# Kernel tuning notes

Measured on AMD Instinct MI355X. Metric: run time of the kernel, lower is better.

## Reference

```python
import jax, jax.numpy as jnp
import numpy as np

D_MODEL = 1024
NUM_HEADS = 16
HEAD_DIM = D_MODEL // NUM_HEADS


def setup_inputs() -> dict:
    key = jax.random.key(0)
    ks = jax.random.split(key, 9)
    s = 1.0 / np.sqrt(D_MODEL)
    return {
        "x": jax.random.normal(ks[0], (4, 2048, D_MODEL), dtype=jnp.float32),
        "Wq": jax.random.uniform(ks[1], (D_MODEL, D_MODEL), minval=-s, maxval=s, dtype=jnp.float32),
        "bq": jax.random.uniform(ks[2], (D_MODEL,), minval=-s, maxval=s, dtype=jnp.float32),
        "Wk": jax.random.uniform(ks[3], (D_MODEL, D_MODEL), minval=-s, maxval=s, dtype=jnp.float32),
        "bk": jax.random.uniform(ks[4], (D_MODEL,), minval=-s, maxval=s, dtype=jnp.float32),
        "Wv": jax.random.uniform(ks[5], (D_MODEL, D_MODEL), minval=-s, maxval=s, dtype=jnp.float32),
        "bv": jax.random.uniform(ks[6], (D_MODEL,), minval=-s, maxval=s, dtype=jnp.float32),
        "Wo": jax.random.uniform(ks[7], (D_MODEL, D_MODEL), minval=-s, maxval=s, dtype=jnp.float32),
        "bo": jax.random.uniform(ks[8], (D_MODEL,), minval=-s, maxval=s, dtype=jnp.float32),
    }


def reference(x, Wq, bq, Wk, bk, Wv, bv, Wo, bo):
    B, T, C = x.shape
    H, Dh = NUM_HEADS, HEAD_DIM
    # projections (nn.Linear applies x @ W^T + b)
    q = (x @ Wq.T + bq).reshape(B, T, H, Dh).transpose(0, 2, 1, 3)  # [B,H,T,Dh]
    k = (x @ Wk.T + bk).reshape(B, T, H, Dh).transpose(0, 2, 1, 3)
    v = (x @ Wv.T + bv).reshape(B, T, H, Dh).transpose(0, 2, 1, 3)
    scale = 1.0 / np.sqrt(Dh).astype(np.float32)
    att = jnp.einsum("bhqd,bhkd->bhqk", q, k) * scale  # [B,H,T,T]
    causal = jnp.tril(jnp.ones((T, T), dtype=bool))
    att = jnp.where(causal[None, None], att, -jnp.inf)
    att = jax.nn.softmax(att, axis=-1)
    # dropout is identity in eval mode
    out = jnp.einsum("bhqk,bhkd->bhqd", att, v)  # [B,H,T,Dh]
    out = out.transpose(0, 2, 1, 3).reshape(B, T, C)
    return out @ Wo.T + bo
```

## Files before the change

### kernel.cpp

```cpp
#include <hip/hip_runtime.h>
#include <stdint.h>

typedef __attribute__((ext_vector_type(8))) short short8;
typedef __attribute__((ext_vector_type(4))) short short4v;
typedef __attribute__((ext_vector_type(4))) float floatx4;

#define QSCALE 0.1803368801111f

__device__ __forceinline__ unsigned short f2bf(float f) {
  unsigned int u = __float_as_uint(f);
  unsigned int r = (u + 0x7FFFu + ((u >> 16) & 1u)) >> 16;
  return (unsigned short)r;
}

__device__ __forceinline__ unsigned int cvt_pk_bf16(float lo, float hi) {
  unsigned int r;
  asm("v_cvt_pk_bf16_f32 %0, %1, %2" : "=v"(r) : "v"(lo), "v"(hi));
  return r;
}

__device__ __forceinline__ void async_copy16(void* lds, const void* g) {
  __builtin_amdgcn_global_load_lds(
      (const __attribute__((address_space(1))) unsigned int*)g,
      (__attribute__((address_space(3))) unsigned int*)lds, 16, 0, 0);
}

__global__ __launch_bounds__(256) void f2b_kernel(const float* __restrict__ in,
                                                  unsigned short* __restrict__ out,
                                                  int n4) {
  int i = blockIdx.x * 256 + threadIdx.x;
  if (i >= n4) return;
  float4 v = ((const float4*)in)[i];
  short4v o;
  o[0] = (short)f2bf(v.x);
  o[1] = (short)f2bf(v.y);
  o[2] = (short)f2bf(v.z);
  o[3] = (short)f2bf(v.w);
  *(short4v*)(out + (long)i * 4) = o;
}

__global__ __launch_bounds__(256) void f2b4_kernel(
    const float* __restrict__ w0, const float* __restrict__ w1,
    const float* __restrict__ w2, const float* __restrict__ w3,
    unsigned short* __restrict__ o0, unsigned short* __restrict__ o1,
    unsigned short* __restrict__ o2, unsigned short* __restrict__ o3) {
  int which = blockIdx.x >> 10;
  const float* in = (which == 0) ? w0 : (which == 1) ? w1 : (which == 2) ? w2 : w3;
  unsigned short* out = (which == 0) ? o0 : (which == 1) ? o1 : (which == 2) ? o2 : o3;
  int i = (blockIdx.x & 1023) * 256 + threadIdx.x;
  float4 v = ((const float4*)in)[i];
  short4v o;
  o[0] = (short)f2bf(v.x);
  o[1] = (short)f2bf(v.y);
  o[2] = (short)f2bf(v.z);
  o[3] = (short)f2bf(v.w);
  *(short4v*)(out + (long)i * 4) = o;
}

__device__ __forceinline__ void gemm128_mainloop(
    const unsigned short* __restrict__ A, const unsigned short* __restrict__ Bt,
    int K, long brow, long bcol, unsigned short* As, unsigned short* Bs,
    floatx4 acc[4][4]) {
  const int tid = threadIdx.x;
  const int wave = tid >> 6;
  const int lane = tid & 63;
  const int wr = wave >> 1, wc = wave & 1;
  const int lr = lane & 15, lg = lane >> 4;

  const unsigned short* ga = A + (brow + (tid >> 2)) * (long)K + (tid & 3) * 8;
  const unsigned short* gb = Bt + (bcol + (tid >> 2)) * (long)K + (tid & 3) * 8;
  unsigned short* lA = As + wave * 512;
  unsigned short* lB = Bs + wave * 512;
  const int a_off = (wr * 64 + lr) * 32 + lg * 8;
  const int b_off = (wc * 64 + lr) * 32 + lg * 8;

  for (int kt = 0; kt < K; kt += 32) {
    __syncthreads();
    async_copy16(lA, ga);
    async_copy16(lA + 2048, ga + (long)64 * K);
    async_copy16(lB, gb);
    async_copy16(lB + 2048, gb + (long)64 * K);
    ga += 32;
    gb += 32;
    __syncthreads();
    short8 af[4], bf[4];
#pragma unroll
    for (int i = 0; i < 4; ++i) {
      af[i] = *(const short8*)(As + a_off + i * 512);
      bf[i] = *(const short8*)(Bs + b_off + i * 512);
    }
#pragma unroll
    for (int i = 0; i < 4; ++i)
#pragma unroll
      for (int j = 0; j < 4; ++j)
        acc[i][j] = __builtin_amdgcn_mfma_f32_16x16x32_bf16(af[i], bf[j], acc[i][j], 0, 0, 0);
  }
}

__global__ __launch_bounds__(256) void qkv_gemm(
    const unsigned short* __restrict__ xb, const unsigned short* __restrict__ wqkv,
    const float* __restrict__ bq, const float* __restrict__ bk,
    const float* __restrict__ bv, unsigned short* __restrict__ q_out,
    unsigned short* __restrict__ k_out, unsigned short* __restrict__ vt_out) {
  __shared__ unsigned short As[128 * 32];
  __shared__ unsigned short Bs[128 * 32];
  floatx4 zero = {0.f, 0.f, 0.f, 0.f};
  floatx4 acc[4][4];
#pragma unroll
  for (int i = 0; i < 4; ++i)
#pragma unroll
    for (int j = 0; j < 4; ++j) acc[i][j] = zero;

  long brow = (long)blockIdx.x * 128;
  long bcol = (long)blockIdx.y * 128;
  gemm128_mainloop(xb, wqkv, 1024, brow, bcol, As, Bs, acc);

  const int wave = threadIdx.x >> 6, lane = threadIdx.x & 63;
  const int wr = wave >> 1, wc = wave & 1, lr = lane & 15, lg = lane >> 4;
  const int kind = (int)(bcol >> 10);
  const float* bias = (kind == 0) ? bq : (kind == 1 ? bk : bv);
#pragma unroll
  for (int i = 0; i < 4; ++i)
#pragma unroll
    for (int j = 0; j < 4; ++j)
#pragma unroll
      for (int r = 0; r < 4; ++r) {
        int m = (int)brow + wr * 64 + i * 16 + lg * 4 + r;
        int n = (int)bcol + wc * 64 + j * 16 + lr;
        int f = n & 1023;
        float v = acc[i][j][r] + bias[f];
        if (kind == 0) v *= QSCALE;
        unsigned short o = f2bf(v);
        int h = f >> 6, d = f & 63;
        int b = m >> 11, t = m & 2047;
        long bh = (long)(b * 16 + h);
        if (kind == 0)
          q_out[(bh * 2048 + t) * 64 + d] = o;
        else if (kind == 1)
          k_out[(bh * 2048 + t) * 64 + d] = o;
        else
          vt_out[(bh * 64 + d) * 2048 + t] = o;
      }
}

__global__ __launch_bounds__(256) void out_gemm(
    const unsigned short* __restrict__ ob, const unsigned short* __restrict__ wo,
    const float* __restrict__ bo, float* __restrict__ out) {
  __shared__ unsigned short As[128 * 32];
  __shared__ unsigned short Bs[128 * 32];
  floatx4 zero = {0.f, 0.f, 0.f, 0.f};
  floatx4 acc[4][4];
#pragma unroll
  for (int i = 0; i < 4; ++i)
#pragma unroll
    for (int j = 0; j < 4; ++j) acc[i][j] = zero;

  long brow = (long)blockIdx.x * 128;
  long bcol = (long)blockIdx.y * 128;
  gemm128_mainloop(ob, wo, 1024, brow, bcol, As, Bs, acc);

  const int wave = threadIdx.x >> 6, lane = threadIdx.x & 63;
  const int wr = wave >> 1, wc = wave & 1, lr = lane & 15, lg = lane >> 4;
#pragma unroll
  for (int i = 0; i < 4; ++i)
#pragma unroll
    for (int j = 0; j < 4; ++j)
#pragma unroll
      for (int r = 0; r < 4; ++r) {
        int m = (int)brow + wr * 64 + i * 16 + lg * 4 + r;
        int n = (int)bcol + wc * 64 + j * 16 + lr;
        out[(long)m * 1024 + n] = acc[i][j][r] + bo[n];
      }
}

__device__ __forceinline__ void stage_kv(char* __restrict__ Kb, char* __restrict__ Vb,
                                         const char* __restrict__ Kp,
                                         const char* __restrict__ Vt, int kv0,
                                         int tid) {
  const int wave = tid >> 6;
#pragma unroll
  for (int j = 0; j < 2; ++j) {
    int d = j * 256 + tid;
    int row = d >> 3, cc = d & 7;
    int gc = cc ^ (row & 7);
    const char* gk = Kp + (size_t)kv0 * 128 + row * 128 + gc * 16;
    async_copy16(Kb + (j * 256 + wave * 64) * 16, gk);
    const char* gv = Vt + (size_t)row * 4096 + (size_t)kv0 * 2 + gc * 16;
    async_copy16(Vb + (j * 256 + wave * 64) * 16, gv);
  }
}

__device__ __forceinline__ void attn_step(
    const char* __restrict__ Kb, const char* __restrict__ Vb,
    char* __restrict__ PTw, const short8 (&qf)[2][2],
    int kv0, int q0, int lr, int lg, bool diag,
    float (&m_i)[2], float (&l_i)[2], floatx4 (&accO)[2][4]) {
  floatx4 zero = {0.f, 0.f, 0.f, 0.f};
  const int x7 = lr & 7;
  floatx4 s[2][4];
  __builtin_amdgcn_s_setprio(1);
#pragma unroll
  for (int nt = 0; nt < 4; ++nt) {
    const char* kr = Kb + (nt * 16 + lr) * 128;
    short8 kf0 = *(const short8*)(kr + ((lg ^ x7) * 16));
    short8 kf1 = *(const short8*)(kr + (((4 + lg) ^ x7) * 16));
#pragma unroll
    for (int qa = 0; qa < 2; ++qa) {
      floatx4 a = zero;
      a = __builtin_amdgcn_mfma_f32_16x16x32_bf16(kf0, qf[qa][0], a, 0, 0, 0);
      a = __builtin_amdgcn_mfma_f32_16x16x32_bf16(kf1, qf[qa][1], a, 0, 0, 0);
      s[qa][nt] = a;
    }
  }
  __builtin_amdgcn_s_setprio(0);

  if (diag) {
#pragma unroll
    for (int qa = 0; qa < 2; ++qa) {
      const int q = q0 + qa * 16 + lr;
#pragma unroll
      for (int nt = 0; nt < 4; ++nt)
#pragma unroll
        for (int r = 0; r < 4; ++r) {
          int kvi = kv0 + nt * 16 + lg * 4 + r;
          if (kvi > q) s[qa][nt][r] = -1e30f;
        }
    }
  }

  float pmax[2];
#pragma unroll
  for (int qa = 0; qa < 2; ++qa) {
    float m0 = fmaxf(fmaxf(s[qa][0][0], s[qa][0][1]), fmaxf(s[qa][0][2], s[qa][0][3]));
    float m1 = fmaxf(fmaxf(s[qa][1][0], s[qa][1][1]), fmaxf(s[qa][1][2], s[qa][1][3]));
    float m2 = fmaxf(fmaxf(s[qa][2][0], s[qa][2][1]), fmaxf(s[qa][2][2], s[qa][2][3]));
    float m3 = fmaxf(fmaxf(s[qa][3][0], s[qa][3][1]), fmaxf(s[qa][3][2], s[qa][3][3]));
    pmax[qa] = fmaxf(fmaxf(m0, m1), fmaxf(m2, m3));
  }

  float g = fmaxf(pmax[0] - m_i[0], pmax[1] - m_i[1]);
  if (__any(g > 11.5f)) {
#pragma unroll
    for (int qa = 0; qa < 2; ++qa) {
      float mx = fmaxf(pmax[qa], __shfl_xor(pmax[qa], 16));
      mx = fmaxf(mx, __shfl_xor(mx, 32));
      float mnew = fmaxf(m_i[qa], mx);
      float scl = exp2f(m_i[qa] - mnew);
      m_i[qa] = mnew;
      l_i[qa] *= scl;
#pragma unroll
      for (int r = 0; r < 4; ++r) {
        float so = __shfl(scl, lg * 4 + r);
#pragma unroll
        for (int dt = 0; dt < 4; ++dt) accO[qa][dt][r] *= so;
      }
    }
  }

#pragma unroll
  for (int qa = 0; qa < 2; ++qa) {
    char* prow = PTw + (qa * 16 + lr) * 128;
#pragma unroll
    for (int nt = 0; nt < 4; ++nt) {
      float p0 = exp2f(s[qa][nt][0] - m_i[qa]);
      float p1 = exp2f(s[qa][nt][1] - m_i[qa]);
      float p2 = exp2f(s[qa][nt][2] - m_i[qa]);
      float p3 = exp2f(s[qa][nt][3] - m_i[qa]);
      l_i[qa] += (p0 + p1) + (p2 + p3);
      uint2 wv;
      wv.x = cvt_pk_bf16(p0, p1);
      wv.y = cvt_pk_bf16(p2, p3);
      *(uint2*)(prow + (((2 * nt + (lg >> 1)) ^ x7) * 16) + ((2 * lg) & 3) * 4) = wv;
    }
  }

  __builtin_amdgcn_s_setprio(1);
#pragma unroll
  for (int kk = 0; kk < 2; ++kk) {
    short8 pf0 = *(const short8*)(PTw + lr * 128 + (((4 * kk + lg) ^ x7) * 16));
    short8 pf1 = *(const short8*)(PTw + (16 + lr) * 128 + (((4 * kk + lg) ^ x7) * 16));
#pragma unroll
    for (int dt = 0; dt < 4; ++dt) {
      short8 vf = *(const short8*)(Vb + (dt * 16 + lr) * 128 + (((4 * kk + lg) ^ x7) * 16));
      accO[0][dt] = __builtin_amdgcn_mfma_f32_16x16x32_bf16(pf0, vf, accO[0][dt], 0, 0, 0);
      accO[1][dt] = __builtin_amdgcn_mfma_f32_16x16x32_bf16(pf1, vf, accO[1][dt], 0, 0, 0);
    }
  }
  __builtin_amdgcn_s_setprio(0);
}

__global__ __launch_bounds__(256, 2) void attn_fwd(
    const unsigned short* __restrict__ qb, const unsigned short* __restrict__ kb,
    const unsigned short* __restrict__ vtb, unsigned short* __restrict__ ob) {
  __shared__ __align__(16) char Kbuf[2][8192];
  __shared__ __align__(16) char Vbuf[2][8192];
  __shared__ __align__(16) char PTbuf[4][4096];

  const int bh = blockIdx.x * 8 + (blockIdx.y & 7);
  const int pr = blockIdx.y >> 3;

  const int tid = threadIdx.x;
  const int wave = tid >> 6, lane = tid & 63;
  const int lr = lane & 15, lg = lane >> 4;
  const unsigned short* Q = qb + (long)bh * 2048 * 64;
  const char* Kp = (const char*)(kb + (long)bh * 2048 * 64);
  const char* Vt = (const char*)(vtb + (long)bh * 64 * 2048);
  const int b = bh >> 4, h = bh & 15;
  char* PTw = PTbuf[wave];

  floatx4 zero = {0.f, 0.f, 0.f, 0.f};

#pragma unroll 1
  for (int half = 0; half < 2; ++half) {
    const int qt = half ? (15 - pr) : pr;
    const int q0 = qt * 128 + wave * 32;
    const int nkv = 2 * qt + 2;

    short8 qf[2][2];
#pragma unroll
    for (int qa = 0; qa < 2; ++qa)
#pragma unroll
      for (int kk = 0; kk < 2; ++kk)
        qf[qa][kk] = *(const short8*)(Q + (q0 + qa * 16 + lr) * 64 + kk * 32 + lg * 8);

    floatx4 accO[2][4];
#pragma unroll
    for (int qa = 0; qa < 2; ++qa)
#pragma unroll
      for (int dt = 0; dt < 4; ++dt) accO[qa][dt] = zero;
    float m_i[2] = {-1e30f, -1e30f};
    float l_i[2] = {0.f, 0.f};

    stage_kv(Kbuf[0], Vbuf[0], Kp, Vt, 0, tid);
    __syncthreads();
#pragma unroll 1
    for (int kv = 0; kv < nkv; ++kv) {
      if (kv + 1 < nkv)
        stage_kv(Kbuf[(kv + 1) & 1], Vbuf[(kv + 1) & 1], Kp, Vt, (kv + 1) * 64, tid);
      attn_step(Kbuf[kv & 1], Vbuf[kv & 1], PTw, qf, kv * 64, q0, lr, lg,
                kv >= 2 * qt, m_i, l_i, accO);
      __syncthreads();
    }

#pragma unroll
    for (int qa = 0; qa < 2; ++qa) {
      float lt = l_i[qa] + __shfl_xor(l_i[qa], 16);
      lt += __shfl_xor(lt, 32);
      float linv = 1.f / lt;
#pragma unroll
      for (int r = 0; r < 4; ++r) {
        float io = __shfl(linv, lg * 4 + r);
        int tq = q0 + qa * 16 + 4 * lg + r;
#pragma unroll
        for (int dt = 0; dt < 4; ++dt)
          ob[((long)b * 2048 + tq) * 1024 + h * 64 + dt * 16 + lr] =
              f2bf(accO[qa][dt][r] * io);
      }
    }
  }
}

extern "C" void kernel_launch(void* const* d_in, const int* in_sizes, int n_in,
                              void* d_out, int out_size, void* d_ws, size_t ws_size,
                              hipStream_t stream) {
  const float* x = (const float*)d_in[0];
  const float* bq = (const float*)d_in[2];
  const float* bk = (const float*)d_in[4];
  const float* bv = (const float*)d_in[6];
  const float* bo = (const float*)d_in[8];
  float* out = (float*)d_out;

  char* ws = (char*)d_ws;
  unsigned short* xb = (unsigned short*)(ws);
  unsigned short* wqkv = (unsigned short*)(ws + (16l << 20));
  unsigned short* wob = (unsigned short*)(ws + (22l << 20));
  unsigned short* qb = (unsigned short*)(ws + (24l << 20));
  unsigned short* kb = (unsigned short*)(ws + (40l << 20));
  unsigned short* vtb = (unsigned short*)(ws + (56l << 20));
  unsigned short* ob = (unsigned short*)(ws + (72l << 20));

  f2b_kernel<<<2097152 / 256, 256, 0, stream>>>(x, xb, 2097152);
  f2b4_kernel<<<4096, 256, 0, stream>>>(
      (const float*)d_in[1], (const float*)d_in[3], (const float*)d_in[5],
      (const float*)d_in[7], wqkv, wqkv + (1l << 20), wqkv + (2l << 20), wob);

  qkv_gemm<<<dim3(64, 24), 256, 0, stream>>>(xb, wqkv, bq, bk, bv, qb, kb, vtb);
  attn_fwd<<<dim3(8, 64), 256, 0, stream>>>(qb, kb, vtb, ob);
  out_gemm<<<dim3(64, 8), 256, 0, stream>>>(ob, wob, bo, out);
}
```

Before: 195.3 us.

## Double-buffer GEMM LDS tiles and merge fp32-to-bf16 conversion kernels

The shared GEMM main loop gets a ping-pong LDS buffer. The next K-tile's async global-to-LDS copy is issued before the MFMAs on the current tile, which drops one of the two barriers per iteration. Both GEMMs get launch_bounds with a minimum of 4 blocks per CU. The separate activation and weight bf16 conversion kernels are merged into one launch to save a kernel launch. The cost is doubled LDS per block, and correctness now depends on the async LDS writes for the next tile completing before the single trailing barrier.

```diff
diff --git a/kernel.cpp b/kernel.cpp
--- a/kernel.cpp
+++ b/kernel.cpp
@@ -25,39 +25,36 @@
       (__attribute__((address_space(3))) unsigned int*)lds, 16, 0, 0);
 }
 
-__global__ __launch_bounds__(256) void f2b_kernel(const float* __restrict__ in,
-                                                  unsigned short* __restrict__ out,
-                                                  int n4) {
-  int i = blockIdx.x * 256 + threadIdx.x;
-  if (i >= n4) return;
+__global__ __launch_bounds__(256) void f2ball_kernel(
+    const float* __restrict__ x, unsigned short* __restrict__ xb,
+    const float* __restrict__ w0, const float* __restrict__ w1,
+    const float* __restrict__ w2, const float* __restrict__ w3,
+    unsigned short* __restrict__ o0, unsigned short* __restrict__ o1,
+    unsigned short* __restrict__ o2, unsigned short* __restrict__ o3) {
+  const float* in;
+  unsigned short* out;
+  long i;
+  if (blockIdx.x < 8192) {
+    in = x;
+    out = xb;
+    i = (long)blockIdx.x * 256 + threadIdx.x;
+  } else {
+    int wb = blockIdx.x - 8192;
+    int which = wb >> 10;
+    in = (which == 0) ? w0 : (which == 1) ? w1 : (which == 2) ? w2 : w3;
+    out = (which == 0) ? o0 : (which == 1) ? o1 : (which == 2) ? o2 : o3;
+    i = (long)(wb & 1023) * 256 + threadIdx.x;
+  }
   float4 v = ((const float4*)in)[i];
   short4v o;
   o[0] = (short)f2bf(v.x);
   o[1] = (short)f2bf(v.y);
   o[2] = (short)f2bf(v.z);
   o[3] = (short)f2bf(v.w);
-  *(short4v*)(out + (long)i * 4) = o;
-}
-
-__global__ __launch_bounds__(256) void f2b4_kernel(
-    const float* __restrict__ w0, const float* __restrict__ w1,
-    const float* __restrict__ w2, const float* __restrict__ w3,
-    unsigned short* __restrict__ o0, unsigned short* __restrict__ o1,
-    unsigned short* __restrict__ o2, unsigned short* __restrict__ o3) {
-  int which = blockIdx.x >> 10;
-  const float* in = (which == 0) ? w0 : (which == 1) ? w1 : (which == 2) ? w2 : w3;
-  unsigned short* out = (which == 0) ? o0 : (which == 1) ? o1 : (which == 2) ? o2 : o3;
-  int i = (blockIdx.x & 1023) * 256 + threadIdx.x;
-  float4 v = ((const float4*)in)[i];
-  short4v o;
-  o[0] = (short)f2bf(v.x);
-  o[1] = (short)f2bf(v.y);
-  o[2] = (short)f2bf(v.z);
-  o[3] = (short)f2bf(v.w);
-  *(short4v*)(out + (long)i * 4) = o;
-}
-
-__device__ __forceinline__ void gemm128_mainloop(
+  *(short4v*)(out + i * 4) = o;
+}
+
+__device__ __forceinline__ void gemm128_mainloop_db(
     const unsigned short* __restrict__ A, const unsigned short* __restrict__ Bt,
     int K, long brow, long bcol, unsigned short* As, unsigned short* Bs,
     floatx4 acc[4][4]) {
@@ -69,41 +66,55 @@
 
   const unsigned short* ga = A + (brow + (tid >> 2)) * (long)K + (tid & 3) * 8;
   const unsigned short* gb = Bt + (bcol + (tid >> 2)) * (long)K + (tid & 3) * 8;
-  unsigned short* lA = As + wave * 512;
-  unsigned short* lB = Bs + wave * 512;
+  const int woff = wave * 512;
   const int a_off = (wr * 64 + lr) * 32 + lg * 8;
   const int b_off = (wc * 64 + lr) * 32 + lg * 8;
 
+  async_copy16(As + woff, ga);
+  async_copy16(As + woff + 2048, ga + (long)64 * K);
+  async_copy16(Bs + woff, gb);
+  async_copy16(Bs + woff + 2048, gb + (long)64 * K);
+  ga += 32;
+  gb += 32;
+  __syncthreads();
+
+  int buf = 0;
   for (int kt = 0; kt < K; kt += 32) {
-    __syncthreads();
-    async_copy16(lA, ga);
-    async_copy16(lA + 2048, ga + (long)64 * K);
-    async_copy16(lB, gb);
-    async_copy16(lB + 2048, gb + (long)64 * K);
-    ga += 32;
-    gb += 32;
-    __syncthreads();
+    if (kt + 32 < K) {
+      unsigned short* lA = As + (buf ^ 1) * 4096 + woff;
+      unsigned short* lB = Bs + (buf ^ 1) * 4096 + woff;
+      async_copy16(lA, ga);
+      async_copy16(lA + 2048, ga + (long)64 * K);
+      async_copy16(lB, gb);
+      async_copy16(lB + 2048, gb + (long)64 * K);
+      ga += 32;
+      gb += 32;
+    }
+    const unsigned short* Ab = As + buf * 4096;
+    const unsigned short* Bb = Bs + buf * 4096;
     short8 af[4], bf[4];
 #pragma unroll
     for (int i = 0; i < 4; ++i) {
-      af[i] = *(const short8*)(As + a_off + i * 512);
-      bf[i] = *(const short8*)(Bs + b_off + i * 512);
+      af[i] = *(const short8*)(Ab + a_off + i * 512);
+      bf[i] = *(const short8*)(Bb + b_off + i * 512);
     }
 #pragma unroll
     for (int i = 0; i < 4; ++i)
 #pragma unroll
       for (int j = 0; j < 4; ++j)
         acc[i][j] = __builtin_amdgcn_mfma_f32_16x16x32_bf16(af[i], bf[j], acc[i][j], 0, 0, 0);
-  }
-}
-
-__global__ __launch_bounds__(256) void qkv_gemm(
+    __syncthreads();
+    buf ^= 1;
+  }
+}
+
+__global__ __launch_bounds__(256, 4) void qkv_gemm(
     const unsigned short* __restrict__ xb, const unsigned short* __restrict__ wqkv,
     const float* __restrict__ bq, const float* __restrict__ bk,
     const float* __restrict__ bv, unsigned short* __restrict__ q_out,
     unsigned short* __restrict__ k_out, unsigned short* __restrict__ vt_out) {
-  __shared__ unsigned short As[128 * 32];
-  __shared__ unsigned short Bs[128 * 32];
+  __shared__ unsigned short As[2 * 128 * 32];
+  __shared__ unsigned short Bs[2 * 128 * 32];
   floatx4 zero = {0.f, 0.f, 0.f, 0.f};
   floatx4 acc[4][4];
 #pragma unroll
@@ -113,7 +124,7 @@
 
   long brow = (long)blockIdx.x * 128;
   long bcol = (long)blockIdx.y * 128;
-  gemm128_mainloop(xb, wqkv, 1024, brow, bcol, As, Bs, acc);
+  gemm128_mainloop_db(xb, wqkv, 1024, brow, bcol, As, Bs, acc);
 
   const int wave = threadIdx.x >> 6, lane = threadIdx.x & 63;
   const int wr = wave >> 1, wc = wave & 1, lr = lane & 15, lg = lane >> 4;
@@ -143,11 +154,11 @@
       }
 }
 
-__global__ __launch_bounds__(256) void out_gemm(
+__global__ __launch_bounds__(256, 4) void out_gemm(
     const unsigned short* __restrict__ ob, const unsigned short* __restrict__ wo,
     const float* __restrict__ bo, float* __restrict__ out) {
-  __shared__ unsigned short As[128 * 32];
-  __shared__ unsigned short Bs[128 * 32];
+  __shared__ unsigned short As[2 * 128 * 32];
+  __shared__ unsigned short Bs[2 * 128 * 32];
   floatx4 zero = {0.f, 0.f, 0.f, 0.f};
   floatx4 acc[4][4];
 #pragma unroll
@@ -157,7 +168,7 @@
 
   long brow = (long)blockIdx.x * 128;
   long bcol = (long)blockIdx.y * 128;
-  gemm128_mainloop(ob, wo, 1024, brow, bcol, As, Bs, acc);
+  gemm128_mainloop_db(ob, wo, 1024, brow, bcol, As, Bs, acc);
 
   const int wave = threadIdx.x >> 6, lane = threadIdx.x & 63;
   const int wr = wave >> 1, wc = wave & 1, lr = lane & 15, lg = lane >> 4;
@@ -379,9 +390,8 @@
   unsigned short* vtb = (unsigned short*)(ws + (56l << 20));
   unsigned short* ob = (unsigned short*)(ws + (72l << 20));
 
-  f2b_kernel<<<2097152 / 256, 256, 0, stream>>>(x, xb, 2097152);
-  f2b4_kernel<<<4096, 256, 0, stream>>>(
-      (const float*)d_in[1], (const float*)d_in[3], (const float*)d_in[5],
+  f2ball_kernel<<<12288, 256, 0, stream>>>(
+      x, xb, (const float*)d_in[1], (const float*)d_in[3], (const float*)d_in[5],
       (const float*)d_in[7], wqkv, wqkv + (1l << 20), wqkv + (2l << 20), wob);
 
   qkv_gemm<<<dim3(64, 24), 256, 0, stream>>>(xb, wqkv, bq, bk, bv, qb, kb, vtb);
```

Result: no change. 192.0 us (-1.7%).
